# Kernel tuning notes

Hardware: AMD Instinct MI355X
Metric: run time of the kernel (lower is better)

The kernel has to match this reference:

```python
import jax, jax.numpy as jnp
import numpy as np

B, C, H, W = 2, 256, 96, 192
GROUPS = 4
K = 9  # search_window_1d = (1, 9) -> 9 candidates, x-offsets -4..4, y-offset 0


def bilinear_sample(img, coords):
    """F.grid_sample(mode='bilinear', padding_mode='zeros', align_corners=True)
    with absolute pixel coordinates (torchvision optical-flow grid_sample wrapper:
    normalize by 2*x/(W-1)-1 then grid_sample align_corners=True == identity mapping).
    img: [B, C, H, W]; coords: [B, Hg, Wg, 2] as (x, y). Returns [B, C, Hg, Wg]."""
    Bi, Ci, Hi, Wi = img.shape
    x = coords[..., 0]
    y = coords[..., 1]
    x0 = jnp.floor(x)
    y0 = jnp.floor(y)
    wx1 = x - x0
    wy1 = y - y0
    wx0 = 1.0 - wx1
    wy0 = 1.0 - wy1
    flat = img.reshape(Bi, Ci, Hi * Wi)

    def gather(ix, iy):
        valid = (ix >= 0) & (ix <= Wi - 1) & (iy >= 0) & (iy <= Hi - 1)
        ixc = jnp.clip(ix, 0, Wi - 1).astype(jnp.int32)
        iyc = jnp.clip(iy, 0, Hi - 1).astype(jnp.int32)
        idx = (iyc * Wi + ixc).reshape(Bi, 1, -1)  # [B,1,Hg*Wg]
        g = jnp.take_along_axis(flat, idx, axis=2)  # [B,C,Hg*Wg]
        g = g.reshape(Bi, Ci, *ix.shape[1:])
        return g * valid[:, None].astype(img.dtype)

    out = (gather(x0, y0) * (wx0 * wy0)[:, None]
           + gather(x0 + 1, y0) * (wx1 * wy0)[:, None]
           + gather(x0, y0 + 1) * (wx0 * wy1)[:, None]
           + gather(x0 + 1, y0 + 1) * (wx1 * wy1)[:, None])
    return out


def setup_inputs() -> dict:
    key = jax.random.key(0)
    k1, k2, k3, k4 = jax.random.split(key, 4)
    return {
        "left_feature": jax.random.normal(k1, (B, C, H, W), dtype=jnp.float32),
        "right_feature": jax.random.normal(k2, (B, C, H, W), dtype=jnp.float32),
        "flow": jax.random.normal(k3, (B, 2, H, W), dtype=jnp.float32),
        "extra_offset": jax.random.normal(k4, (B, 2 * K, H, W), dtype=jnp.float32),
    }


def reference(left_feature, right_feature, flow, extra_offset):
    Bf, Cf, Hf, Wf = left_feature.shape
    gc = Cf // GROUPS
    dt = left_feature.dtype
    # 1d window offsets: meshgrid(arange(-4,5), arange(0,1), 'xy') -> (x, 0) pairs
    xs = jnp.arange(-4, 5, dtype=dt)
    win_offs = jnp.stack([xs, jnp.zeros_like(xs)], axis=-1)  # [K,2] (x,y)
    # extra_offset: [B, K, 2, H, W] -> [B, K, H, W, 2]
    extra = extra_offset.reshape(Bf, K, 2, Hf, Wf).transpose(0, 1, 3, 4, 2)
    offsets = win_offs[None, :, None, None, :] + extra  # [B,K,H,W,2]
    # base coords grid (x, y) + flow
    yy, xx = jnp.meshgrid(jnp.arange(Hf), jnp.arange(Wf), indexing="ij")
    base = jnp.stack([xx, yy], axis=-1).astype(dt)  # [H,W,2]
    coords = base[None] + flow.transpose(0, 2, 3, 1)  # [B,H,W,2]
    coords = coords[:, None] + offsets  # [B,K,H,W,2]
    coords = coords.reshape(Bf, K * Hf, Wf, 2)
    # All groups share identical window/dilation -> sample full right feature once.
    sampled = bilinear_sample(right_feature, coords)  # [B,C,K*H,W]
    sampled = sampled.reshape(Bf, GROUPS, gc, K, Hf, Wf)
    left = left_feature.reshape(Bf, GROUPS, gc, 1, Hf, Wf)
    corr = jnp.mean(left * sampled, axis=2)  # [B,G,K,H,W]
    return corr.reshape(Bf, GROUPS * K, Hf, Wf)
```

## Files before the change

### kernel.cpp

```cpp
#include <hip/hip_runtime.h>


namespace {
constexpr int kB = 2;
constexpr int kC = 256;
constexpr int kH = 96;
constexpr int kW = 192;
constexpr int kG = 4;
constexpr int kGC = kC / kG;
constexpr int kK = 9;
constexpr int kHW = kH * kW;
constexpr size_t kPlane = (size_t)kC * kHW;
constexpr int kTransBlocks = (kHW / 64) * (kC / 64) * kB;
constexpr int kPx = 16;
constexpr int kCorrBlocks  = kB * kHW / kPx;
}

typedef _Float16 half8_t __attribute__((ext_vector_type(8)));
typedef _Float16 half2_t __attribute__((ext_vector_type(2)));

struct TapMeta {
  int4   off;
  float4 wgt;
};

__device__ __forceinline__ float dot8(half8_t a, half8_t b, float acc) {
#if __has_builtin(__builtin_amdgcn_fdot2)
  #pragma unroll
  for (int i = 0; i < 4; ++i) {
    half2_t a2 = {a[2 * i], a[2 * i + 1]};
    half2_t b2 = {b[2 * i], b[2 * i + 1]};
    acc = __builtin_amdgcn_fdot2(a2, b2, acc, false);
  }
#else
  #pragma unroll
  for (int i = 0; i < 8; ++i) acc += (float)a[i] * (float)b[i];
#endif
  return acc;
}

__global__ __launch_bounds__(256) void prepass_kernel(
    const float* __restrict__ right, _Float16* __restrict__ right_t)
{
  __shared__ float tile[64][65];
  int tb = blockIdx.x;
  int pt = tb % (kHW / 64);
  int ct = (tb / (kHW / 64)) % 4;
  int b  = tb / ((kHW / 64) * 4);
  int p0 = pt * 64, c0 = ct * 64;
  const float* inb = right + (size_t)b * kPlane;
  _Float16*   outb = right_t + (size_t)b * kPlane;
  int t = threadIdx.x;
  int cl = t >> 2;
  int q  = t & 3;
  #pragma unroll
  for (int i = 0; i < 4; ++i) {
    int j = q + 4 * i;
    float4 v = *(const float4*)(inb + (size_t)(c0 + cl) * kHW + p0 + 4 * j);
    tile[cl][4 * j + 0] = v.x;
    tile[cl][4 * j + 1] = v.y;
    tile[cl][4 * j + 2] = v.z;
    tile[cl][4 * j + 3] = v.w;
  }
  __syncthreads();
  int pl8 = t >> 3;
  int c8  = t & 7;
  #pragma unroll
  for (int i = 0; i < 2; ++i) {
    int px = pl8 + 32 * i;
    half8_t hv;
    #pragma unroll
    for (int j = 0; j < 8; ++j)
      hv[j] = (_Float16)tile[8 * c8 + j][px];
    *(half8_t*)(outb + (size_t)(p0 + px) * kC + c0 + 8 * c8) = hv;
  }
}

__global__ __launch_bounds__(512, 4) void corr_fp16_kernel(
    const _Float16* __restrict__ right_t, const float* __restrict__ left,
    const float* __restrict__ flow, const float* __restrict__ extra,
    float* __restrict__ out)
{
  __shared__ _Float16 smleft[kPx][kC];
  __shared__ float    smflow[20][kPx];
  __shared__ TapMeta  smeta[kPx * kK];
  __shared__ float    smout[kG * kK][kPx];

  int sb = (blockIdx.x & 7) * (kCorrBlocks / 8) + (blockIdx.x >> 3);
  int blockPix = sb * kPx;
  int b    = blockPix / kHW;
  int pix0 = blockPix % kHW;

  int t = threadIdx.x;

  #pragma unroll
  for (int it = 0; it < 2; ++it) {
    int c = (t >> 2) + 128 * it;
    int q = t & 3;
    float4 v = *(const float4*)(left + (size_t)b * kPlane +
                                (size_t)c * kHW + pix0 + 4 * q);
    smleft[4 * q + 0][c] = (_Float16)v.x;
    smleft[4 * q + 1][c] = (_Float16)v.y;
    smleft[4 * q + 2][c] = (_Float16)v.z;
    smleft[4 * q + 3][c] = (_Float16)v.w;
  }

  if (t < 320) {
    int fr = t >> 4, fpx = t & 15;
    const float* src = (fr < 2)
        ? flow  + ((size_t)b * 2  + fr)       * kHW + pix0 + fpx
        : extra + ((size_t)b * 18 + (fr - 2)) * kHW + pix0 + fpx;
    smflow[fr][fpx] = *src;
  }
  __syncthreads();

  if (t < kPx * kK) {
    int px = t / kK;
    int k  = t - px * kK;
    int gpix = pix0 + px;
    int w = gpix % kW, h = gpix / kW;

    float bx = (float)w + smflow[0][px];
    float by = (float)h + smflow[1][px];
    float xx = bx + (float)(k - 4) + smflow[2 + 2 * k][px];
    float yy = by + smflow[2 + 2 * k + 1][px];
    float xf = floorf(xx), yf = floorf(yy);
    float fx = xx - xf, fy = yy - yf;
    int ix0 = (int)xf, iy0 = (int)yf;
    int ix1 = ix0 + 1, iy1 = iy0 + 1;
    bool vx0 = (ix0 >= 0) && (ix0 < kW);
    bool vx1 = (ix1 >= 0) && (ix1 < kW);
    bool vy0 = (iy0 >= 0) && (iy0 < kH);
    bool vy1 = (iy1 >= 0) && (iy1 < kH);
    int xc0 = min(max(ix0, 0), kW - 1);
    int xc1 = min(max(ix1, 0), kW - 1);
    int yc0 = min(max(iy0, 0), kH - 1);
    int yc1 = min(max(iy1, 0), kH - 1);
    float wx0 = 1.f - fx, wy0 = 1.f - fy;
    TapMeta m;
    m.off.x = (yc0 * kW + xc0) * kC;
    m.off.y = (yc0 * kW + xc1) * kC;
    m.off.z = (yc1 * kW + xc0) * kC;
    m.off.w = (yc1 * kW + xc1) * kC;
    m.wgt.x = wx0 * wy0 * ((vx0 && vy0) ? 1.f : 0.f);
    m.wgt.y = fx  * wy0 * ((vx1 && vy0) ? 1.f : 0.f);
    m.wgt.z = wx0 * fy  * ((vx0 && vy1) ? 1.f : 0.f);
    m.wgt.w = fx  * fy  * ((vx1 && vy1) ? 1.f : 0.f);
    smeta[t] = m;
  }

  int wv   = t >> 6;
  int lane = t & 63;
  int p    = lane >> 5;
  int cl   = lane & 31;
  int px   = wv * 2 + p;

  const _Float16* Rb = right_t + (size_t)b * kPlane + cl * 8;

  __syncthreads();

  half8_t l8 = *(const half8_t*)&smleft[px][cl * 8];
  const TapMeta* mp = smeta + px * kK;

  float rr[kK];
  half8_t tA[12], tB[12];

#define LOAD_TAPS(T, KB) do {                                      \
    int4 o0 = mp[(KB)].off, o1 = mp[(KB) + 1].off, o2 = mp[(KB) + 2].off; \
    T[0]  = *(const half8_t*)(Rb + o0.x);                          \
    T[1]  = *(const half8_t*)(Rb + o0.y);                          \
    T[2]  = *(const half8_t*)(Rb + o0.z);                          \
    T[3]  = *(const half8_t*)(Rb + o0.w);                          \
    T[4]  = *(const half8_t*)(Rb + o1.x);                          \
    T[5]  = *(const half8_t*)(Rb + o1.y);                          \
    T[6]  = *(const half8_t*)(Rb + o1.z);                          \
    T[7]  = *(const half8_t*)(Rb + o1.w);                          \
    T[8]  = *(const half8_t*)(Rb + o2.x);                          \
    T[9]  = *(const half8_t*)(Rb + o2.y);                          \
    T[10] = *(const half8_t*)(Rb + o2.z);                          \
    T[11] = *(const half8_t*)(Rb + o2.w);                          \
  } while (0)

#define COMP_TAPS(T, KB) do {                                      \
    _Pragma("unroll")                                              \
    for (int j = 0; j < 3; ++j) {                                  \
      float4 w4 = mp[(KB) + j].wgt;                                \
      float d00 = dot8(T[4 * j + 0], l8, 0.f);                     \
      float d01 = dot8(T[4 * j + 1], l8, 0.f);                     \
      float d10 = dot8(T[4 * j + 2], l8, 0.f);                     \
      float d11 = dot8(T[4 * j + 3], l8, 0.f);                     \
      float r = w4.x * d00 + w4.y * d01 + w4.z * d10 + w4.w * d11; \
      r += __shfl_xor(r, 1);                                       \
      r += __shfl_xor(r, 2);                                       \
      r += __shfl_xor(r, 4);                                       \
      rr[(KB) + j] = r;                                            \
    }                                                              \
  } while (0)

  LOAD_TAPS(tA, 0);
  LOAD_TAPS(tB, 3);
  __builtin_amdgcn_sched_barrier(0);
  COMP_TAPS(tA, 0);
  LOAD_TAPS(tA, 6);
  __builtin_amdgcn_sched_barrier(0);
  COMP_TAPS(tB, 3);
  COMP_TAPS(tA, 6);

#undef LOAD_TAPS
#undef COMP_TAPS

  if ((cl & 7) == 0) {
    int g = cl >> 3;
    #pragma unroll
    for (int k = 0; k < kK; ++k)
      smout[g * kK + k][px] = rr[k] * (1.f / kGC);
  }
  __syncthreads();
  {
    float* ob = out + (size_t)b * kG * kK * kHW + pix0;
    int r   = t >> 4;
    int px2 = t & 15;
    ob[(size_t)r * kHW + px2] = smout[r][px2];
    if (t < (kG * kK - 32) * kPx) {
      int r2 = 32 + (t >> 4);
      ob[(size_t)r2 * kHW + px2] = smout[r2][px2];
    }
  }
}

__global__ __launch_bounds__(256) void crestereo_corr_fallback(
    const float* __restrict__ left, const float* __restrict__ right,
    const float* __restrict__ flow, const float* __restrict__ extra,
    float* __restrict__ out)
{
  int t = blockIdx.x * blockDim.x + threadIdx.x;
  int w = t % kW;
  int h = (t / kW) % kH;
  int k = (t / kHW) % kK;
  int g = (t / (kHW * kK)) % kG;
  int b = t / (kHW * kK * kG);

  int pix = h * kW + w;
  const float* flowb = flow + b * 2 * kHW + pix;
  float x = (float)(w + (k - 4)) + flowb[0];
  float y = (float)h + flowb[kHW];
  const float* extb = extra + (size_t)(b * 2 * kK + 2 * k) * kHW + pix;
  x += extb[0];
  y += extb[kHW];

  float xf = floorf(x), yf = floorf(y);
  float fx = x - xf, fy = y - yf;
  int ix0 = (int)xf, iy0 = (int)yf;
  int ix1 = ix0 + 1, iy1 = iy0 + 1;
  bool vx0 = (ix0 >= 0) && (ix0 < kW);
  bool vx1 = (ix1 >= 0) && (ix1 < kW);
  bool vy0 = (iy0 >= 0) && (iy0 < kH);
  bool vy1 = (iy1 >= 0) && (iy1 < kH);
  int xc0 = min(max(ix0, 0), kW - 1);
  int xc1 = min(max(ix1, 0), kW - 1);
  int yc0 = min(max(iy0, 0), kH - 1);
  int yc1 = min(max(iy1, 0), kH - 1);
  float wx0 = 1.f - fx, wy0 = 1.f - fy;
  float w00 = wx0 * wy0 * ((vx0 && vy0) ? 1.f : 0.f);
  float w01 = fx  * wy0 * ((vx1 && vy0) ? 1.f : 0.f);
  float w10 = wx0 * fy  * ((vx0 && vy1) ? 1.f : 0.f);
  float w11 = fx  * fy  * ((vx1 && vy1) ? 1.f : 0.f);
  int idx = yc0 * kW + xc0;
  int dx  = xc1 - xc0;
  int dyw = (yc1 - yc0) * kW;

  const float* Rb = right + (size_t)(b * kC + g * kGC) * kHW + idx;
  const float* Lb = left  + (size_t)(b * kC + g * kGC) * kHW + pix;

  float acc = 0.f;
  #pragma unroll 4
  for (int c = 0; c < kGC; ++c) {
    const float* Rc = Rb + (size_t)c * kHW;
    float l   = Lb[(size_t)c * kHW];
    acc += l * (w00 * Rc[0] + w01 * Rc[dx] + w10 * Rc[dyw] + w11 * Rc[dx + dyw]);
  }
  out[(size_t)((b * kG + g) * kK + k) * kHW + pix] = acc * (1.f / kGC);
}

extern "C" void kernel_launch(void* const* d_in, const int* in_sizes, int n_in,
                              void* d_out, int out_size, void* d_ws, size_t ws_size,
                              hipStream_t stream) {
  const float* left  = (const float*)d_in[0];
  const float* right = (const float*)d_in[1];
  const float* flow  = (const float*)d_in[2];
  const float* extra = (const float*)d_in[3];
  float* out = (float*)d_out;

  size_t t_bytes = (size_t)kB * kPlane * sizeof(_Float16);
  if (ws_size >= t_bytes) {
    _Float16* right_t = (_Float16*)d_ws;

    prepass_kernel<<<kTransBlocks, 256, 0, stream>>>(right, right_t);
    corr_fp16_kernel<<<kCorrBlocks, 512, 0, stream>>>(
        right_t, left, flow, extra, out);
  } else {
    int total = kB * kG * kK * kH * kW;
    crestereo_corr_fallback<<<(total + 255) / 256, 256, 0, stream>>>(
        left, right, flow, extra, out);
  }
}
```

Before: 136.9 us.

## Use inline-asm gather loads with manual vmcnt waits and a third tap buffer

Replaces the compiler-generated tap gathers with inline-asm global_load_dwordx4 and explicit s_waitcnt vmcnt(12) counters. Loads for the next tap group stay in flight while the current group is computed, and a third register buffer lets the last group's loads be issued before the second group is consumed. Occupancy in launch bounds is lowered from 4 to 2 waves per SIMD to make room for the extra 48 VGPRs. The risks are fewer resident waves to hide gather latency, and hand-written waitcnt values that become incorrect if the compiler inserts other vector memory ops.

```diff
diff --git a/kernel.cpp b/kernel.cpp
--- a/kernel.cpp
+++ b/kernel.cpp
@@ -37,6 +37,13 @@
   for (int i = 0; i < 8; ++i) acc += (float)a[i] * (float)b[i];
 #endif
   return acc;
+}
+
+__device__ __forceinline__ half8_t ld16(const _Float16* p) {
+  half8_t r;
+  asm volatile("global_load_dwordx4 %0, %1, off"
+               : "=&v"(r) : "v"(p));
+  return r;
 }
 
 __global__ __launch_bounds__(256) void prepass_kernel(
@@ -76,7 +83,7 @@
   }
 }
 
-__global__ __launch_bounds__(512, 4) void corr_fp16_kernel(
+__global__ __launch_bounds__(512, 2) void corr_fp16_kernel(
     const _Float16* __restrict__ right_t, const float* __restrict__ left,
     const float* __restrict__ flow, const float* __restrict__ extra,
     float* __restrict__ out)
@@ -163,22 +170,22 @@
   const TapMeta* mp = smeta + px * kK;
 
   float rr[kK];
-  half8_t tA[12], tB[12];
-
-#define LOAD_TAPS(T, KB) do {                                      \
+  half8_t tA[12], tB[12], tC[12];
+
+#define ISSUE_TAPS(T, KB) do {                                           \
     int4 o0 = mp[(KB)].off, o1 = mp[(KB) + 1].off, o2 = mp[(KB) + 2].off; \
-    T[0]  = *(const half8_t*)(Rb + o0.x);                          \
-    T[1]  = *(const half8_t*)(Rb + o0.y);                          \
-    T[2]  = *(const half8_t*)(Rb + o0.z);                          \
-    T[3]  = *(const half8_t*)(Rb + o0.w);                          \
-    T[4]  = *(const half8_t*)(Rb + o1.x);                          \
-    T[5]  = *(const half8_t*)(Rb + o1.y);                          \
-    T[6]  = *(const half8_t*)(Rb + o1.z);                          \
-    T[7]  = *(const half8_t*)(Rb + o1.w);                          \
-    T[8]  = *(const half8_t*)(Rb + o2.x);                          \
-    T[9]  = *(const half8_t*)(Rb + o2.y);                          \
-    T[10] = *(const half8_t*)(Rb + o2.z);                          \
-    T[11] = *(const half8_t*)(Rb + o2.w);                          \
+    T[0]  = ld16(Rb + o0.x);                                             \
+    T[1]  = ld16(Rb + o0.y);                                             \
+    T[2]  = ld16(Rb + o0.z);                                             \
+    T[3]  = ld16(Rb + o0.w);                                             \
+    T[4]  = ld16(Rb + o1.x);                                             \
+    T[5]  = ld16(Rb + o1.y);                                             \
+    T[6]  = ld16(Rb + o1.z);                                             \
+    T[7]  = ld16(Rb + o1.w);                                             \
+    T[8]  = ld16(Rb + o2.x);                                             \
+    T[9]  = ld16(Rb + o2.y);                                             \
+    T[10] = ld16(Rb + o2.z);                                             \
+    T[11] = ld16(Rb + o2.w);                                             \
   } while (0)
 
 #define COMP_TAPS(T, KB) do {                                      \
@@ -197,16 +204,20 @@
     }                                                              \
   } while (0)
 
-  LOAD_TAPS(tA, 0);
-  LOAD_TAPS(tB, 3);
+  ISSUE_TAPS(tA, 0);
+  ISSUE_TAPS(tB, 3);
+  asm volatile("s_waitcnt vmcnt(12)" ::: "memory");
   __builtin_amdgcn_sched_barrier(0);
   COMP_TAPS(tA, 0);
-  LOAD_TAPS(tA, 6);
+  ISSUE_TAPS(tC, 6);
+  asm volatile("s_waitcnt vmcnt(12)" ::: "memory");
   __builtin_amdgcn_sched_barrier(0);
   COMP_TAPS(tB, 3);
-  COMP_TAPS(tA, 6);
-
-#undef LOAD_TAPS
+  asm volatile("s_waitcnt vmcnt(0)" ::: "memory");
+  __builtin_amdgcn_sched_barrier(0);
+  COMP_TAPS(tC, 6);
+
+#undef ISSUE_TAPS
 #undef COMP_TAPS
 
   if ((cl & 7) == 0) {
```

Result: no change. 134.6 us, median of 2 (-1.7%).
